# Kernel tuning notes

Hardware: AMD Instinct MI355X
Metric: run time of the kernel (lower is better)

The kernel has to match this reference:

```python
import jax, jax.numpy as jnp
import numpy as np

B, HW, C = 128, 1024, 384

def setup_inputs() -> dict:
    key = jax.random.key(0)
    k1, k2, k3 = jax.random.split(key, 3)
    x = jax.random.normal(k1, (B, HW + 1, C), dtype=jnp.float32)
    cls_token = jax.random.normal(k2, (B, 1, C), dtype=jnp.float32)
    edge_aggregation = jax.random.normal(k3, (B, HW, C), dtype=jnp.float32)
    return {"x": x, "cls_token": cls_token, "edge_aggregation": edge_aggregation, "pool": 1}


def reference(x, cls_token, edge_aggregation, pool):
    # edge_aggregation: (B, HW, C) -> avgpool over HW -> (B, 1, C)
    ea = jnp.mean(edge_aggregation, axis=1, keepdims=True)
    channel_importance = jax.nn.sigmoid(ea)                      # (B, 1, C)
    nodes = x[:, 1:]                                             # (B, HW, C)
    # channel_aggregation: nodes @ channel_importance^T -> (B, HW, 1)
    channel_aggregation = jnp.einsum('bnc,bc->bn', nodes, channel_importance[:, 0])[..., None]
    node_importance = jax.nn.sigmoid(channel_aggregation)        # (B, HW, 1)
    # node_aggregation: node_importance^T @ nodes -> (B, 1, C)
    node_aggregation = jnp.einsum('bn,bnc->bc', node_importance[..., 0], nodes)[:, None, :]
    # global (Frobenius) 2-norms, matching torch .norm(2) over the whole tensor
    normalization = jnp.linalg.norm(cls_token) / jnp.linalg.norm(node_aggregation)
    cls_token_out = cls_token + normalization * node_aggregation  # (B, 1, C)
    if pool:
        # ascending sort by channel_aggregation, keep top quarter (largest importance)
        idx = jnp.argsort(channel_aggregation[..., 0], axis=1)    # (B, HW)
        nodes_sorted = jnp.take_along_axis(nodes, idx[..., None], axis=1)
        hw = nodes.shape[1]
        nodes_pooled = nodes_sorted[:, hw // 4 * 3:]              # (B, HW/4, C)
        out = jnp.concatenate([cls_token_out, nodes_pooled], axis=1)
    else:
        out = jnp.concatenate([cls_token_out, nodes], axis=1)
    return out
```

## Files before the change

### kernel.cpp

```cpp
#include <hip/hip_runtime.h>
#include <math.h>

#define B 128
#define N 1024
#define C 384
#define C4 96
#define XROWS 1025
#define OUTROWS 257

typedef float f32x4 __attribute__((ext_vector_type(4)));

#define OFF_NA   0
#define SZ_NA    (B * C)
#define OFF_SQ   (OFF_NA + SZ_NA)
#define SZ_SQ    (2 * B)

__device__ __forceinline__ float sigmoidf(float v) { return 1.f / (1.f + expf(-v)); }
__device__ __forceinline__ float dot4v(f32x4 a, f32x4 b) {
    return a.x * b.x + a.y * b.y + a.z * b.z + a.w * b.w;
}

__global__ __launch_bounds__(1024) void fatk(const float* __restrict__ x,
                                             const float* __restrict__ cls,
                                             const float* __restrict__ ea,
                                             float* __restrict__ na,
                                             float* __restrict__ sqp,
                                             float* __restrict__ out) {
    int b = blockIdx.x, tid = threadIdx.x;
    int w = tid >> 6, lane = tid & 63, hl = lane & 31, half = lane >> 5;

    __shared__ float sci[C];
    __shared__ float dots[N];
    __shared__ f32x4 sacc[16][C4];
    __shared__ unsigned long long bufA[N];
    __shared__ unsigned long long bufB[N];
    __shared__ unsigned llist[256];
    __shared__ float escr[2 * C4];

    {
        const float* eb = ea + (size_t)b * N * C;
        f32x4 eacc[3];
#pragma unroll
        for (int k = 0; k < 3; ++k) eacc[k] = (f32x4)(0.f);
#pragma unroll 2
        for (int it = 0; it < 32; ++it) {
            int r = 32 * it + 2 * w + half;
            const f32x4* rp = (const f32x4*)(eb + (size_t)r * C);
#pragma unroll
            for (int k = 0; k < 3; ++k)
                eacc[k] += __builtin_nontemporal_load(&rp[hl + 32 * k]);
        }
#pragma unroll
        for (int k = 0; k < 3; ++k) {
            eacc[k].x += __shfl_xor(eacc[k].x, 32, 64);
            eacc[k].y += __shfl_xor(eacc[k].y, 32, 64);
            eacc[k].z += __shfl_xor(eacc[k].z, 32, 64);
            eacc[k].w += __shfl_xor(eacc[k].w, 32, 64);
        }
        if (half == 0) {
#pragma unroll
            for (int k = 0; k < 3; ++k) sacc[w][hl + 32 * k] = eacc[k];
        }
    }
    __syncthreads();
    if (tid < C4) {
        f32x4 s = (f32x4)(0.f);
#pragma unroll
        for (int w2 = 0; w2 < 16; ++w2) s += sacc[w2][tid];
        s *= (1.f / (float)N);
        sci[4 * tid + 0] = sigmoidf(s.x);
        sci[4 * tid + 1] = sigmoidf(s.y);
        sci[4 * tid + 2] = sigmoidf(s.z);
        sci[4 * tid + 3] = sigmoidf(s.w);
    }
    __syncthreads();

    f32x4 cir[3];
#pragma unroll
    for (int k = 0; k < 3; ++k) cir[k] = ((const f32x4*)sci)[hl + 32 * k];
    f32x4 acc[3];
#pragma unroll
    for (int k = 0; k < 3; ++k) acc[k] = (f32x4)(0.f);

    const float* xb = x + (size_t)b * XROWS * C + C;
#pragma unroll 2
    for (int it = 0; it < 32; ++it) {
        int r = 32 * it + 2 * w + half;
        const f32x4* rp = (const f32x4*)(xb + (size_t)r * C);
        f32x4 v[3];
        float dotv = 0.f;
#pragma unroll
        for (int k = 0; k < 3; ++k) {
            v[k] = rp[hl + 32 * k];
            dotv += dot4v(v[k], cir[k]);
        }
#pragma unroll
        for (int off = 16; off > 0; off >>= 1) dotv += __shfl_xor(dotv, off, 64);
        if (hl == 0) dots[r] = dotv;
        float si = sigmoidf(dotv);
#pragma unroll
        for (int k = 0; k < 3; ++k) acc[k] += si * v[k];
    }
#pragma unroll
    for (int k = 0; k < 3; ++k) {
        acc[k].x += __shfl_xor(acc[k].x, 32, 64);
        acc[k].y += __shfl_xor(acc[k].y, 32, 64);
        acc[k].z += __shfl_xor(acc[k].z, 32, 64);
        acc[k].w += __shfl_xor(acc[k].w, 32, 64);
    }
    if (half == 0) {
#pragma unroll
        for (int k = 0; k < 3; ++k) sacc[w][hl + 32 * k] = acc[k];
    }
    __syncthreads();

    if (tid < C4) {
        f32x4 s = (f32x4)(0.f);
#pragma unroll
        for (int w2 = 0; w2 < 16; ++w2) s += sacc[w2][tid];
        ((f32x4*)(na + (size_t)b * C))[tid] = s;
        escr[tid] = dot4v(s, s);
        f32x4 cv = ((const f32x4*)(cls + (size_t)b * C))[tid];
        escr[C4 + tid] = dot4v(cv, cv);
    }
    __syncthreads();
    if (w == 0) {
        float nss = (lane < 32) ? (escr[lane] + escr[lane + 32] + escr[lane + 64]) : 0.f;
        float css = (lane < 32) ? (escr[C4 + lane] + escr[C4 + lane + 32] + escr[C4 + lane + 64]) : 0.f;
#pragma unroll
        for (int off = 32; off > 0; off >>= 1) {
            nss += __shfl_xor(nss, off, 64);
            css += __shfl_xor(css, off, 64);
        }
        if (lane == 0) { sqp[b] = nss; sqp[B + b] = css; }
    }

    float vv = dots[tid];
    unsigned u = __float_as_uint(vv);
    u = (u & 0x80000000u) ? ~u : (u | 0x80000000u);
    unsigned long long key = ((unsigned long long)u << 32) | (unsigned)tid;

    bool useA = true;
    for (int k = 2; k <= N; k <<= 1) {
        bool up = ((tid & k) == 0);
        for (int j = k >> 1; j > 0; j >>= 1) {
            unsigned long long other;
            if (j < 64) {
                other = __shfl_xor(key, j, 64);
            } else {
                unsigned long long* buf = useA ? bufA : bufB;
                useA = !useA;
                buf[tid] = key;
                __syncthreads();
                other = buf[tid ^ j];
            }
            bool iAmLow = ((tid & j) == 0);
            bool keepMin = (iAmLow == up);
            bool otherLess = (other < key);
            key = (keepMin == otherLess) ? other : key;
        }
    }
    __syncthreads();

    unsigned* flag = (unsigned*)bufA;
    unsigned* wsum = (unsigned*)bufB;
    flag[tid] = 0;
    __syncthreads();
    if (tid >= 768) flag[(unsigned)(key & 1023u)] = (unsigned)(tid - 768) | 0x80000000u;
    __syncthreads();
    unsigned f = flag[tid];
    bool sel = (f & 0x80000000u) != 0;
    unsigned long long bal = __ballot(sel);
    if (lane == 0) wsum[w] = (unsigned)__popcll(bal);
    __syncthreads();
    if (sel) {
        int base = 0;
        for (int w2 = 0; w2 < w; ++w2) base += (int)wsum[w2];
        int intra = (int)__popcll(bal & ((1ull << lane) - 1ull));
        llist[base + intra] = ((unsigned)tid << 8) | (f & 0xFFu);
    }
    __syncthreads();

    const float* xb2 = x + ((size_t)b * XROWS + 1) * C;
#pragma unroll 4
    for (int q = 0; q < 24; ++q) {
        int e = tid + 1024 * q;
        int lp = e / C4, c4 = e % C4;
        unsigned ent = llist[lp];
        int node = (int)(ent >> 8);
        int op = (int)(ent & 0xFFu);
        f32x4 sv = *((const f32x4*)(xb2 + (size_t)node * C) + c4);
        __builtin_nontemporal_store(sv,
            (f32x4*)(out + ((size_t)b * OUTROWS + 1 + op) * C) + c4);
    }
}

__global__ __launch_bounds__(384) void kZ_cls(const float* __restrict__ sqp,
                                              const float* __restrict__ cls,
                                              const float* __restrict__ na,
                                              float* __restrict__ out) {
    int b = blockIdx.x, t = threadIdx.x;
    __shared__ float2 red[128];
    if (t < 128) red[t] = make_float2(sqp[t], sqp[B + t]);
    __syncthreads();
    for (int o = 64; o > 0; o >>= 1) {
        if (t < o) {
            float2 a = red[t], d = red[t + o];
            red[t] = make_float2(a.x + d.x, a.y + d.y);
        }
        __syncthreads();
    }
    float ratio = sqrtf(red[0].y / red[0].x);
    out[((size_t)b * OUTROWS) * C + t] =
        cls[(size_t)b * C + t] + ratio * na[(size_t)b * C + t];
}

extern "C" void kernel_launch(void* const* d_in, const int* in_sizes, int n_in,
                              void* d_out, int out_size, void* d_ws, size_t ws_size,
                              hipStream_t stream) {
    const float* x   = (const float*)d_in[0];
    const float* cls = (const float*)d_in[1];
    const float* ea  = (const float*)d_in[2];
    float* out = (float*)d_out;
    float* ws  = (float*)d_ws;

    float* na  = ws + OFF_NA;
    float* sqp = ws + OFF_SQ;

    fatk<<<B, 1024, 0, stream>>>(x, cls, ea, na, sqp, out);
    kZ_cls<<<B, 384, 0, stream>>>(sqp, cls, na, out);
}
```

Before: 92.69 us.

## Split each batch across two cooperating blocks and fuse cls-token kernel via last-block

Launches two 1024-thread blocks per batch item instead of one, each handling half the rows for the edge mean and node aggregation. The halves exchange partial sums and dot products through global memory with atomic flag spin-waits. Both blocks run the full sort redundantly and each gathers half of the selected rows. The second kernel is removed: the last block to finish, found with an atomic counter, computes the global norm ratio and writes the cls rows. This is meant to double the number of blocks on the device for better CU utilisation and to remove a launch. It adds inter-block spin synchronisation that relies on both blocks of a pair being co-resident, a memset per call, and a serial cls tail in one block.

```diff
diff --git a/kernel.cpp b/kernel.cpp
--- a/kernel.cpp
+++ b/kernel.cpp
@@ -10,40 +10,63 @@
 
 typedef float f32x4 __attribute__((ext_vector_type(4)));
 
-#define OFF_NA   0
-#define SZ_NA    (B * C)
-#define OFF_SQ   (OFF_NA + SZ_NA)
-#define SZ_SQ    (2 * B)
+#define OFF_FLAGS 0
+#define OFF_EAP   512
+#define SZ_EAP    (B * 2 * C)
+#define OFF_NAPH  (OFF_EAP + SZ_EAP)
+#define SZ_NAPH   (B * C)
+#define OFF_NA    (OFF_NAPH + SZ_NAPH)
+#define SZ_NA     (B * C)
+#define OFF_SQ    (OFF_NA + SZ_NA)
+#define SZ_SQ     (2 * B)
+#define OFF_DOTS  (OFF_SQ + SZ_SQ)
+#define SZ_DOTS   (B * N)
 
 __device__ __forceinline__ float sigmoidf(float v) { return 1.f / (1.f + expf(-v)); }
 __device__ __forceinline__ float dot4v(f32x4 a, f32x4 b) {
     return a.x * b.x + a.y * b.y + a.z * b.z + a.w * b.w;
 }
-
-__global__ __launch_bounds__(1024) void fatk(const float* __restrict__ x,
+__device__ __forceinline__ void st_ag(float* p, float v) {
+    __hip_atomic_store(p, v, __ATOMIC_RELAXED, __HIP_MEMORY_SCOPE_AGENT);
+}
+__device__ __forceinline__ float ld_ag(const float* p) {
+    return __hip_atomic_load(p, __ATOMIC_RELAXED, __HIP_MEMORY_SCOPE_AGENT);
+}
+
+__global__ __launch_bounds__(1024) void fat2(const float* __restrict__ x,
                                              const float* __restrict__ cls,
                                              const float* __restrict__ ea,
+                                             int* __restrict__ flags,
+                                             float* __restrict__ eaP,
+                                             float* __restrict__ naPh,
                                              float* __restrict__ na,
                                              float* __restrict__ sqp,
+                                             float* __restrict__ dotsG,
                                              float* __restrict__ out) {
-    int b = blockIdx.x, tid = threadIdx.x;
+    int b = blockIdx.x, g = blockIdx.y, tid = threadIdx.x;
     int w = tid >> 6, lane = tid & 63, hl = lane & 31, half = lane >> 5;
 
     __shared__ float sci[C];
-    __shared__ float dots[N];
+    __shared__ float dotsL[512];
     __shared__ f32x4 sacc[16][C4];
     __shared__ unsigned long long bufA[N];
     __shared__ unsigned long long bufB[N];
     __shared__ unsigned llist[256];
     __shared__ float escr[2 * C4];
+    __shared__ int lastB;
+    if (tid == 0) lastB = 0;
+
+    int* flagEA = flags;
+    int* flagX  = flags + B;
+    int* done   = flags + 2 * B;
 
     {
-        const float* eb = ea + (size_t)b * N * C;
+        const float* eb = ea + ((size_t)b * N + (size_t)g * 512) * C;
         f32x4 eacc[3];
 #pragma unroll
         for (int k = 0; k < 3; ++k) eacc[k] = (f32x4)(0.f);
 #pragma unroll 2
-        for (int it = 0; it < 32; ++it) {
+        for (int it = 0; it < 16; ++it) {
             int r = 32 * it + 2 * w + half;
             const f32x4* rp = (const f32x4*)(eb + (size_t)r * C);
 #pragma unroll
@@ -63,15 +86,32 @@
         }
     }
     __syncthreads();
+    f32x4 s0 = (f32x4)(0.f);
     if (tid < C4) {
-        f32x4 s = (f32x4)(0.f);
-#pragma unroll
-        for (int w2 = 0; w2 < 16; ++w2) s += sacc[w2][tid];
-        s *= (1.f / (float)N);
-        sci[4 * tid + 0] = sigmoidf(s.x);
-        sci[4 * tid + 1] = sigmoidf(s.y);
-        sci[4 * tid + 2] = sigmoidf(s.z);
-        sci[4 * tid + 3] = sigmoidf(s.w);
+#pragma unroll
+        for (int w2 = 0; w2 < 16; ++w2) s0 += sacc[w2][tid];
+        float* pe = &eaP[((size_t)b * 2 + g) * C + 4 * tid];
+        st_ag(pe + 0, s0.x); st_ag(pe + 1, s0.y);
+        st_ag(pe + 2, s0.z); st_ag(pe + 3, s0.w);
+    }
+    __syncthreads();
+    if (tid == 0) {
+        __threadfence();
+        __hip_atomic_fetch_add(flagEA + b, 1, __ATOMIC_RELEASE, __HIP_MEMORY_SCOPE_AGENT);
+        while (__hip_atomic_load(flagEA + b, __ATOMIC_ACQUIRE, __HIP_MEMORY_SCOPE_AGENT) < 2)
+            __builtin_amdgcn_s_sleep(1);
+    }
+    __syncthreads();
+    if (tid < C4) {
+        const float* pe = &eaP[((size_t)b * 2 + (1 - g)) * C + 4 * tid];
+        f32x4 sp;
+        sp.x = ld_ag(pe + 0); sp.y = ld_ag(pe + 1);
+        sp.z = ld_ag(pe + 2); sp.w = ld_ag(pe + 3);
+        f32x4 m = (s0 + sp) * (1.f / (float)N);
+        sci[4 * tid + 0] = sigmoidf(m.x);
+        sci[4 * tid + 1] = sigmoidf(m.y);
+        sci[4 * tid + 2] = sigmoidf(m.z);
+        sci[4 * tid + 3] = sigmoidf(m.w);
     }
     __syncthreads();
 
@@ -82,9 +122,9 @@
 #pragma unroll
     for (int k = 0; k < 3; ++k) acc[k] = (f32x4)(0.f);
 
-    const float* xb = x + (size_t)b * XROWS * C + C;
+    const float* xb = x + (size_t)b * XROWS * C + C + (size_t)g * 512 * C;
 #pragma unroll 2
-    for (int it = 0; it < 32; ++it) {
+    for (int it = 0; it < 16; ++it) {
         int r = 32 * it + 2 * w + half;
         const f32x4* rp = (const f32x4*)(xb + (size_t)r * C);
         f32x4 v[3];
@@ -96,7 +136,10 @@
         }
 #pragma unroll
         for (int off = 16; off > 0; off >>= 1) dotv += __shfl_xor(dotv, off, 64);
-        if (hl == 0) dots[r] = dotv;
+        if (hl == 0) {
+            dotsL[r] = dotv;
+            st_ag(&dotsG[(size_t)b * N + g * 512 + r], dotv);
+        }
         float si = sigmoidf(dotv);
 #pragma unroll
         for (int k = 0; k < 3; ++k) acc[k] += si * v[k];
@@ -113,29 +156,57 @@
         for (int k = 0; k < 3; ++k) sacc[w][hl + 32 * k] = acc[k];
     }
     __syncthreads();
-
+    f32x4 sNA = (f32x4)(0.f);
     if (tid < C4) {
-        f32x4 s = (f32x4)(0.f);
-#pragma unroll
-        for (int w2 = 0; w2 < 16; ++w2) s += sacc[w2][tid];
-        ((f32x4*)(na + (size_t)b * C))[tid] = s;
-        escr[tid] = dot4v(s, s);
-        f32x4 cv = ((const f32x4*)(cls + (size_t)b * C))[tid];
-        escr[C4 + tid] = dot4v(cv, cv);
-    }
-    __syncthreads();
-    if (w == 0) {
-        float nss = (lane < 32) ? (escr[lane] + escr[lane + 32] + escr[lane + 64]) : 0.f;
-        float css = (lane < 32) ? (escr[C4 + lane] + escr[C4 + lane + 32] + escr[C4 + lane + 64]) : 0.f;
-#pragma unroll
-        for (int off = 32; off > 0; off >>= 1) {
-            nss += __shfl_xor(nss, off, 64);
-            css += __shfl_xor(css, off, 64);
-        }
-        if (lane == 0) { sqp[b] = nss; sqp[B + b] = css; }
-    }
-
-    float vv = dots[tid];
+#pragma unroll
+        for (int w2 = 0; w2 < 16; ++w2) sNA += sacc[w2][tid];
+        if (g == 1) {
+            float* pn = &naPh[(size_t)b * C + 4 * tid];
+            st_ag(pn + 0, sNA.x); st_ag(pn + 1, sNA.y);
+            st_ag(pn + 2, sNA.z); st_ag(pn + 3, sNA.w);
+        }
+    }
+    __syncthreads();
+    if (tid == 0) {
+        __threadfence();
+        __hip_atomic_fetch_add(flagX + b, 1, __ATOMIC_RELEASE, __HIP_MEMORY_SCOPE_AGENT);
+        while (__hip_atomic_load(flagX + b, __ATOMIC_ACQUIRE, __HIP_MEMORY_SCOPE_AGENT) < 2)
+            __builtin_amdgcn_s_sleep(1);
+    }
+    __syncthreads();
+
+    if (g == 0) {
+        if (tid < C4) {
+            const float* pn = &naPh[(size_t)b * C + 4 * tid];
+            sNA.x += ld_ag(pn + 0); sNA.y += ld_ag(pn + 1);
+            sNA.z += ld_ag(pn + 2); sNA.w += ld_ag(pn + 3);
+            float* po = &na[(size_t)b * C + 4 * tid];
+            st_ag(po + 0, sNA.x); st_ag(po + 1, sNA.y);
+            st_ag(po + 2, sNA.z); st_ag(po + 3, sNA.w);
+            escr[tid] = dot4v(sNA, sNA);
+            f32x4 cv = ((const f32x4*)(cls + (size_t)b * C))[tid];
+            escr[C4 + tid] = dot4v(cv, cv);
+        }
+        __syncthreads();
+        if (w == 0) {
+            float nss = (lane < 32) ? (escr[lane] + escr[lane + 32] + escr[lane + 64]) : 0.f;
+            float css = (lane < 32) ? (escr[C4 + lane] + escr[C4 + lane + 32] + escr[C4 + lane + 64]) : 0.f;
+#pragma unroll
+            for (int off = 32; off > 0; off >>= 1) {
+                nss += __shfl_xor(nss, off, 64);
+                css += __shfl_xor(css, off, 64);
+            }
+            if (lane == 0) { st_ag(&sqp[b], nss); st_ag(&sqp[B + b], css); }
+        }
+        __syncthreads();
+        if (tid == 0) {
+            __threadfence();
+            int old = __hip_atomic_fetch_add(done, 1, __ATOMIC_ACQ_REL, __HIP_MEMORY_SCOPE_AGENT);
+            if (old == B - 1) lastB = 1;
+        }
+    }
+
+    float vv = ((tid >> 9) == g) ? dotsL[tid & 511] : ld_ag(&dotsG[(size_t)b * N + tid]);
     unsigned u = __float_as_uint(vv);
     u = (u & 0x80000000u) ? ~u : (u | 0x80000000u);
     unsigned long long key = ((unsigned long long)u << 32) | (unsigned)tid;
@@ -183,9 +254,9 @@
 
     const float* xb2 = x + ((size_t)b * XROWS + 1) * C;
 #pragma unroll 4
-    for (int q = 0; q < 24; ++q) {
+    for (int q = 0; q < 12; ++q) {
         int e = tid + 1024 * q;
-        int lp = e / C4, c4 = e % C4;
+        int lp = 128 * g + e / C4, c4 = e % C4;
         unsigned ent = llist[lp];
         int node = (int)(ent >> 8);
         int op = (int)(ent & 0xFFu);
@@ -193,26 +264,26 @@
         __builtin_nontemporal_store(sv,
             (f32x4*)(out + ((size_t)b * OUTROWS + 1 + op) * C) + c4);
     }
-}
-
-__global__ __launch_bounds__(384) void kZ_cls(const float* __restrict__ sqp,
-                                              const float* __restrict__ cls,
-                                              const float* __restrict__ na,
-                                              float* __restrict__ out) {
-    int b = blockIdx.x, t = threadIdx.x;
-    __shared__ float2 red[128];
-    if (t < 128) red[t] = make_float2(sqp[t], sqp[B + t]);
-    __syncthreads();
-    for (int o = 64; o > 0; o >>= 1) {
-        if (t < o) {
-            float2 a = red[t], d = red[t + o];
-            red[t] = make_float2(a.x + d.x, a.y + d.y);
+
+    __syncthreads();
+    if (lastB) {
+        if (tid < 128) {
+            dotsL[tid]       = ld_ag(&sqp[tid]);
+            dotsL[256 + tid] = ld_ag(&sqp[B + tid]);
         }
         __syncthreads();
-    }
-    float ratio = sqrtf(red[0].y / red[0].x);
-    out[((size_t)b * OUTROWS) * C + t] =
-        cls[(size_t)b * C + t] + ratio * na[(size_t)b * C + t];
+        if (tid == 0) {
+            float nss = 0.f, css = 0.f;
+            for (int i = 0; i < 128; ++i) { nss += dotsL[i]; css += dotsL[256 + i]; }
+            escr[0] = sqrtf(css / nss);
+        }
+        __syncthreads();
+        float ratio = escr[0];
+        for (int e = tid; e < B * C; e += 1024) {
+            int bb = e / C, c = e - bb * C;
+            out[(size_t)bb * OUTROWS * C + c] = cls[e] + ratio * ld_ag(&na[e]);
+        }
+    }
 }
 
 extern "C" void kernel_launch(void* const* d_in, const int* in_sizes, int n_in,
@@ -224,9 +295,13 @@
     float* out = (float*)d_out;
     float* ws  = (float*)d_ws;
 
-    float* na  = ws + OFF_NA;
-    float* sqp = ws + OFF_SQ;
-
-    fatk<<<B, 1024, 0, stream>>>(x, cls, ea, na, sqp, out);
-    kZ_cls<<<B, 384, 0, stream>>>(sqp, cls, na, out);
-}
+    int*   flags = (int*)ws;
+    float* eaP   = ws + OFF_EAP;
+    float* naPh  = ws + OFF_NAPH;
+    float* na    = ws + OFF_NA;
+    float* sqp   = ws + OFF_SQ;
+    float* dotsG = ws + OFF_DOTS;
+
+    hipMemsetAsync(flags, 0, 2048, stream);
+    fat2<<<dim3(B, 2), 1024, 0, stream>>>(x, cls, ea, flags, eaP, naPh, na, sqp, dotsG, out);
+}
```

Measured after the change: 127.6 us. 37.7% more time.
